# Performance work log

Measured on AMD Instinct MI355X. Metric: run time of the kernel, lower is better.

Reference implementation:

```python
import jax, jax.numpy as jnp
import numpy as np
from jax import lax

L, H, C, V, BLK = 6, 12, 768, 50257, 1024
B, T = 4, 1024
HD = C // H
EPS = 1e-5


def _norm(key, shape, scale=0.02):
    return jax.random.normal(key, shape, dtype=jnp.float32) * scale


def setup_inputs() -> dict:
    key = jax.random.key(0)
    ks = jax.random.split(key, 16)
    idx = jax.random.randint(ks[0], (B, T), 0, V)
    inp = {
        "idx": idx,
        "wte": _norm(ks[1], (V, C)),
        "wpe": _norm(ks[2], (BLK, C)),
        "ln1_s": jnp.ones((L, C)),
        "ln1_b": jnp.zeros((L, C)),
        "qkv_w": _norm(ks[3], (L, C, 3 * C)),
        "qkv_b": jnp.zeros((L, 3 * C)),
        "proj_w": _norm(ks[4], (L, C, C)),
        "proj_b": jnp.zeros((L, C)),
        "ln2_s": jnp.ones((L, C)),
        "ln2_b": jnp.zeros((L, C)),
        "fc_w": _norm(ks[5], (L, C, 4 * C)),
        "fc_b": jnp.zeros((L, 4 * C)),
        "fcp_w": _norm(ks[6], (L, 4 * C, C)),
        "fcp_b": jnp.zeros((L, C)),
        "lnf_s": jnp.ones((C,)),
        "lnf_b": jnp.zeros((C,)),
    }
    return inp


def layer_norm(x, s, b):
    mu = jnp.mean(x, axis=-1, keepdims=True)
    var = jnp.mean(jnp.square(x - mu), axis=-1, keepdims=True)
    return (x - mu) * lax.rsqrt(var + EPS) * s + b


def block(x, p):
    ln1_s, ln1_b, qkv_w, qkv_b, proj_w, proj_b, ln2_s, ln2_b, fc_w, fc_b, fcp_w, fcp_b = p
    Bx, Tx, Cx = x.shape
    h = layer_norm(x, ln1_s, ln1_b)
    qkv = h @ qkv_w + qkv_b  # [B,T,3C]
    q, k, v = jnp.split(qkv, 3, axis=-1)
    q = q.reshape(Bx, Tx, H, HD).swapaxes(1, 2)  # [B,H,T,hd]
    k = k.reshape(Bx, Tx, H, HD).swapaxes(1, 2)
    v = v.reshape(Bx, Tx, H, HD).swapaxes(1, 2)
    attn = jnp.einsum("bhqd,bhkd->bhqk", q, k) / jnp.sqrt(jnp.float32(HD))
    mask = jnp.tril(jnp.ones((Tx, Tx), dtype=bool))
    attn = jnp.where(mask, attn, -jnp.inf)
    attn = jax.nn.softmax(attn, axis=-1)
    y = jnp.einsum("bhqk,bhkd->bhqd", attn, v)
    y = y.swapaxes(1, 2).reshape(Bx, Tx, Cx)
    x = x + (y @ proj_w + proj_b)
    h = layer_norm(x, ln2_s, ln2_b)
    h = jax.nn.gelu(h @ fc_w + fc_b, approximate=True)
    x = x + (h @ fcp_w + fcp_b)
    return x


def reference(idx, wte, wpe, ln1_s, ln1_b, qkv_w, qkv_b, proj_w, proj_b,
              ln2_s, ln2_b, fc_w, fc_b, fcp_w, fcp_b, lnf_s, lnf_b):
    Tx = idx.shape[1]
    x = wte[idx] + wpe[:Tx][None]  # [B,T,C]
    params = (ln1_s, ln1_b, qkv_w, qkv_b, proj_w, proj_b,
              ln2_s, ln2_b, fc_w, fc_b, fcp_w, fcp_b)
    def step(carry, p):
        return block(carry, p), None
    x, _ = lax.scan(step, x, params)
    x = layer_norm(x, lnf_s, lnf_b)
    logits = x @ wte.T  # tied embedding attend
    return logits
```

## Files before the change

### kernel.cpp

```cpp
#include <hip/hip_runtime.h>
#include <math.h>

#define LNUM 6
#define HNUM 12
#define CDIM 768
#define VDIM 50257
#define BDIM 4
#define TDIM 1024
#define NTOK 4096

typedef __bf16 bf16;
typedef __bf16 bf16x8 __attribute__((ext_vector_type(8)));
typedef float  floatx4 __attribute__((ext_vector_type(4)));
typedef unsigned int u32;

__device__ inline void gload16(const bf16* gsrc, bf16* lds) {
  __builtin_amdgcn_global_load_lds(
      (const __attribute__((address_space(1))) u32*)gsrc,
      (__attribute__((address_space(3))) u32*)lds, 16, 0, 0);
}

__global__ void k_cvt_bf16(const float* __restrict__ in, bf16* __restrict__ out, long n) {
  long i = ((long)blockIdx.x * blockDim.x + threadIdx.x) * 4;
  long stride = (long)gridDim.x * blockDim.x * 4;
  for (; i < n; i += stride) {
    float4 v = *reinterpret_cast<const float4*>(in + i);
    bf16 b0 = (bf16)v.x, b1 = (bf16)v.y, b2 = (bf16)v.z, b3 = (bf16)v.w;
    ushort4 pk;
    pk.x = __builtin_bit_cast(unsigned short, b0);
    pk.y = __builtin_bit_cast(unsigned short, b1);
    pk.z = __builtin_bit_cast(unsigned short, b2);
    pk.w = __builtin_bit_cast(unsigned short, b3);
    *reinterpret_cast<ushort4*>(out + i) = pk;
  }
}

#define TILES_QKV  1728
#define TILES_PROJ 576
#define TILES_FC   2304
#define TILES_FCP  2304
#define TILES_LAYER (TILES_QKV + TILES_PROJ + TILES_FC + TILES_FCP)

__global__ __launch_bounds__(256) void k_trans_all(
    const float* __restrict__ qkv_w, const float* __restrict__ proj_w,
    const float* __restrict__ fc_w, const float* __restrict__ fcp_w,
    bf16* __restrict__ wq, bf16* __restrict__ wp,
    bf16* __restrict__ wf, bf16* __restrict__ wfp) {
  __shared__ float tile[32][33];
  int bid = blockIdx.x;
  int layer = bid / TILES_LAYER, r = bid % TILES_LAYER;
  const float* src; bf16* dst; int K, N, tx, ty;
  if (r < TILES_QKV) {
    src = qkv_w + (size_t)layer * CDIM * 3 * CDIM; dst = wq + (size_t)layer * CDIM * 3 * CDIM;
    K = CDIM; N = 3 * CDIM; tx = r % 72; ty = r / 72;
  } else if (r < TILES_QKV + TILES_PROJ) {
    r -= TILES_QKV;
    src = proj_w + (size_t)layer * CDIM * CDIM; dst = wp + (size_t)layer * CDIM * CDIM;
    K = CDIM; N = CDIM; tx = r % 24; ty = r / 24;
  } else if (r < TILES_QKV + TILES_PROJ + TILES_FC) {
    r -= TILES_QKV + TILES_PROJ;
    src = fc_w + (size_t)layer * CDIM * 4 * CDIM; dst = wf + (size_t)layer * CDIM * 4 * CDIM;
    K = CDIM; N = 4 * CDIM; tx = r % 96; ty = r / 96;
  } else {
    r -= TILES_QKV + TILES_PROJ + TILES_FC;
    src = fcp_w + (size_t)layer * 4 * CDIM * CDIM; dst = wfp + (size_t)layer * 4 * CDIM * CDIM;
    K = 4 * CDIM; N = CDIM; tx = r % 24; ty = r / 24;
  }
  int n0 = tx * 32, k0 = ty * 32;
  int nx = threadIdx.x & 31, tyy = threadIdx.x >> 5;
  #pragma unroll
  for (int p = 0; p < 4; ++p) {
    int k = tyy + p * 8;
    tile[k][nx] = src[(size_t)(k0 + k) * N + n0 + nx];
  }
  __syncthreads();
  #pragma unroll
  for (int p = 0; p < 4; ++p) {
    int n = tyy + p * 8;
    dst[(size_t)(n0 + n) * K + k0 + nx] = (bf16)tile[nx][n];
  }
}

__global__ void k_embed(const int* __restrict__ idx, const float* __restrict__ wte,
                        const float* __restrict__ wpe, float* __restrict__ x) {
  int tok = blockIdx.x;
  int t = tok & (TDIM - 1);
  int id = idx[tok];
  const float* a = wte + (size_t)id * CDIM;
  const float* p = wpe + (size_t)t * CDIM;
  float* o = x + (size_t)tok * CDIM;
  for (int c = threadIdx.x; c < CDIM; c += 256) o[c] = a[c] + p[c];
}

__global__ __launch_bounds__(256) void k_layernorm(const float* __restrict__ x,
    const float* __restrict__ sc, const float* __restrict__ bi, bf16* __restrict__ out) {
  __shared__ float red[8];
  int row = blockIdx.x;
  const float* xr = x + (size_t)row * CDIM;
  int t = threadIdx.x;
  float v0 = xr[t], v1 = xr[t + 256], v2 = xr[t + 512];
  float s = v0 + v1 + v2;
  #pragma unroll
  for (int o = 32; o > 0; o >>= 1) s += __shfl_down(s, o);
  if ((t & 63) == 0) red[t >> 6] = s;
  __syncthreads();
  float mean = (red[0] + red[1] + red[2] + red[3]) * (1.0f / CDIM);
  float d0 = v0 - mean, d1 = v1 - mean, d2 = v2 - mean;
  float q = d0 * d0 + d1 * d1 + d2 * d2;
  #pragma unroll
  for (int o = 32; o > 0; o >>= 1) q += __shfl_down(q, o);
  if ((t & 63) == 0) red[4 + (t >> 6)] = q;
  __syncthreads();
  float var = (red[4] + red[5] + red[6] + red[7]) * (1.0f / CDIM);
  float rs = rsqrtf(var + 1e-5f);
  bf16* orow = out + (size_t)row * CDIM;
  orow[t]       = (bf16)(d0 * rs * sc[t]       + bi[t]);
  orow[t + 256] = (bf16)(d1 * rs * sc[t + 256] + bi[t + 256]);
  orow[t + 512] = (bf16)(d2 * rs * sc[t + 512] + bi[t + 512]);
}

__device__ inline float gelu_f(float x) {
  float x3 = x * x * x;
  return 0.5f * x * (1.0f + tanhf(0.7978845608028654f * (x + 0.044715f * x3)));
}

template<int TBM, int EPI>
__global__ __launch_bounds__(512, 1) void k_gemm8(
    const bf16* __restrict__ A, const bf16* __restrict__ Bt,
    const float* __restrict__ bias,
    float* __restrict__ Cf, bf16* __restrict__ Cb,
    int N, int K) {
  constexpr int MI = TBM / 32;
  constexpr int MH = MI / 2;
  constexpr int MTILES = 4096 / TBM;
  __shared__ __align__(16) bf16 smem[2 * 8192 + 2 * TBM * 32];
  bf16* Bs = smem;
  bf16* As = smem + 2 * 8192;
  const int nwg = gridDim.x;
  const int id = blockIdx.x;
  const int swz = (id & 7) * (nwg >> 3) + (id >> 3);
  const int m0 = (swz % MTILES) * TBM;
  const int n0 = (swz / MTILES) * 256;
  const int tid = threadIdx.x, lane = tid & 63, wave = tid >> 6;
  const int wr = wave >> 2, wc = wave & 3;
  const int g = lane >> 4, r16 = lane & 15;
  const int numK = K >> 5;
  const int wsl = wave * 512;

  const int srow = wave * 16 + (lane >> 2);
  const int scol = ((lane & 3) ^ ((lane >> 3) & 3)) * 8;
  const bf16* at  = A  + (size_t)(m0 + srow) * K + scol;
  const bf16* at1 = A  + (size_t)(m0 + srow + 128) * K + scol;
  const bf16* bt  = Bt + (size_t)(n0 + srow) * K + scol;
  const bf16* bt1 = Bt + (size_t)(n0 + srow + 128) * K + scol;
  const int sw = (g ^ ((r16 >> 1) & 3)) * 8;
  const int a_off = (wr * (TBM / 2) + r16) * 32 + sw;
  const int b_off = (wc * 64 + r16) * 32 + sw;

  floatx4 acc[MI][4] = {};

#define STB(s0, s1, pb) do { gload16((s0), Bs + (pb) * 8192 + wsl); \
                             gload16((s1), Bs + (pb) * 8192 + wsl + 4096); } while (0)
#define STA(s0, s1, pb) do { gload16((s0), As + (pb) * TBM * 32 + wsl); \
                             if constexpr (TBM == 256) gload16((s1), As + (pb) * TBM * 32 + wsl + 4096); } while (0)

  STB(bt, bt1, 0);
  STA(at, at1, 0);
  STB(bt + 32, bt1 + 32, 1);
  asm volatile("s_waitcnt vmcnt(2)" ::: "memory");
  __builtin_amdgcn_s_barrier();

  for (int t = 0; t < numK; ++t) {
    const int p = t & 1, pn = p ^ 1;
    bf16x8 af[MH], bfr[4];

    #pragma unroll
    for (int j = 0; j < 4; ++j) bfr[j] = *(const bf16x8*)&Bs[p * 8192 + b_off + j * 512];
    #pragma unroll
    for (int i = 0; i < MH; ++i) af[i] = *(const bf16x8*)&As[p * TBM * 32 + a_off + i * 512];
    if (t + 1 < numK) STA(at + 32, at1 + 32, pn);
    __builtin_amdgcn_s_barrier();
    asm volatile("s_waitcnt lgkmcnt(0)" ::: "memory");
    __builtin_amdgcn_s_setprio(1);
    #pragma unroll
    for (int i = 0; i < MH; ++i)
      #pragma unroll
      for (int j = 0; j < 4; ++j)
        acc[i][j] = __builtin_amdgcn_mfma_f32_16x16x32_bf16(af[i], bfr[j], acc[i][j], 0, 0, 0);
    __builtin_amdgcn_s_setprio(0);
    __builtin_amdgcn_s_barrier();

    #pragma unroll
    for (int i = 0; i < MH; ++i) af[i] = *(const bf16x8*)&As[p * TBM * 32 + a_off + (i + MH) * 512];
    if (t + 2 < numK) STB(bt + 64, bt1 + 64, p);
    __builtin_amdgcn_s_barrier();
    asm volatile("s_waitcnt lgkmcnt(0)" ::: "memory");
    __builtin_amdgcn_s_setprio(1);
    #pragma unroll
    for (int i = 0; i < MH; ++i)
      #pragma unroll
      for (int j = 0; j < 4; ++j)
        acc[i + MH][j] = __builtin_amdgcn_mfma_f32_16x16x32_bf16(af[i], bfr[j], acc[i + MH][j], 0, 0, 0);
    __builtin_amdgcn_s_setprio(0);
    if (t + 2 < numK) { asm volatile("s_waitcnt vmcnt(2)" ::: "memory"); }
    else              { asm volatile("s_waitcnt vmcnt(0)" ::: "memory"); }
    __builtin_amdgcn_s_barrier();

    at += 32; at1 += 32; bt += 32; bt1 += 32;
  }
#undef STB
#undef STA

  if (EPI == 0) {
    float* sb = reinterpret_cast<float*>(smem) + wave * 1088;
    const int seg = lane & 15, rq = lane >> 4;
    const int mrow_base = m0 + wr * (TBM / 2);
    const int ncol_base = n0 + wc * 64;
    #pragma unroll
    for (int mf = 0; mf < MI; ++mf) {
      #pragma unroll
      for (int nf = 0; nf < 4; ++nf) {
        #pragma unroll
        for (int q = 0; q < 4; ++q)
          sb[(g * 4 + q) * 68 + nf * 16 + r16] = acc[mf][nf][q];
      }
      #pragma unroll
      for (int pz = 0; pz < 4; ++pz) {
        int row = rq + pz * 4;
        floatx4 v = *reinterpret_cast<const floatx4*>(&sb[row * 68 + seg * 4]);
        int m = mrow_base + mf * 16 + row;
        int n = ncol_base + seg * 4;
        if (n + 4 <= N) {
          __builtin_memcpy(&Cf[(size_t)m * N + n], &v, 16);
        } else {
          #pragma unroll
          for (int e = 0; e < 4; ++e)
            if (n + e < N) Cf[(size_t)m * N + n + e] = v[e];
        }
      }
    }
  } else {
    bf16* sb = smem + wave * 1152;
    const int rr_rd = lane & 15, seg = lane >> 4;
    const int nb = n0 + wc * 64 + r16;
    float bv[4];
    #pragma unroll
    for (int j = 0; j < 4; ++j) bv[j] = bias[nb + j * 16];
    #pragma unroll
    for (int mf = 0; mf < MI; ++mf) {
      #pragma unroll
      for (int j = 0; j < 4; ++j) {
        #pragma unroll
        for (int q = 0; q < 4; ++q) {
          float v = acc[mf][j][q] + bv[j];
          if (EPI == 3) v = gelu_f(v);
          sb[(g * 4 + q) * 72 + j * 16 + r16] = (bf16)v;
        }
      }
      bf16x8 o0 = *(const bf16x8*)&sb[rr_rd * 72 + seg * 16];
      bf16x8 o1 = *(const bf16x8*)&sb[rr_rd * 72 + seg * 16 + 8];
      size_t orow = (size_t)(m0 + wr * (TBM / 2) + mf * 16 + rr_rd) * N + (n0 + wc * 64 + seg * 16);
      *(bf16x8*)&Cb[orow] = o0;
      *(bf16x8*)&Cb[orow + 8] = o1;
    }
  }
}

template<int TBM, int MI, int NI, int EPI>
__global__ __launch_bounds__(256) void k_gemm(
    const bf16* __restrict__ A, const bf16* __restrict__ Bt,
    const float* __restrict__ bias, const float* __restrict__ resid,
    float* __restrict__ Cf, bf16* __restrict__ Cb,
    int M, int N, int K) {
  constexpr int BN = 128;
  constexpr int WGN = BN / (NI * 16);
  constexpr int AI = TBM / 32;
  constexpr int BI = BN / 32;
  __shared__ __align__(16) bf16 As[TBM * 64];
  __shared__ __align__(16) bf16 Bs[BN * 64];
  const int m0 = blockIdx.x * TBM, n0 = blockIdx.y * BN;
  const int tid = threadIdx.x;
  const int lane = tid & 63, wave = tid >> 6;
  const int wr = wave / WGN, wc = wave % WGN;
  const int l8 = lane >> 3, s8 = lane & 7;
  const int g = lane >> 4, r16 = lane & 15;

  floatx4 acc[MI][NI] = {};

  const bf16* a_src = A + (size_t)(m0 + l8) * K + s8 * 8;
  const bf16* b_src = Bt + (size_t)(n0 + l8) * K + s8 * 8;

  for (int k0 = 0; k0 < K; k0 += 64) {
    #pragma unroll
    for (int t = 0; t < AI; ++t) {
      int row0 = wave * (TBM / 4) + t * 8;
      gload16(a_src + (size_t)row0 * K + k0, &As[row0 * 64]);
    }
    #pragma unroll
    for (int t = 0; t < BI; ++t) {
      int row0 = wave * 32 + t * 8;
      gload16(b_src + (size_t)row0 * K + k0, &Bs[row0 * 64]);
    }
    __syncthreads();
    #pragma unroll
    for (int kk = 0; kk < 2; ++kk) {
      bf16x8 af[MI], bfr[NI];
      #pragma unroll
      for (int i = 0; i < MI; ++i)
        af[i] = *reinterpret_cast<const bf16x8*>(&As[(wr * MI * 16 + i * 16 + r16) * 64 + g * 8 + kk * 32]);
      #pragma unroll
      for (int j = 0; j < NI; ++j)
        bfr[j] = *reinterpret_cast<const bf16x8*>(&Bs[(wc * NI * 16 + j * 16 + r16) * 64 + g * 8 + kk * 32]);
      #pragma unroll
      for (int i = 0; i < MI; ++i) {
        #pragma unroll
        for (int j = 0; j < NI; ++j)
          acc[i][j] = __builtin_amdgcn_mfma_f32_16x16x32_bf16(af[i], bfr[j], acc[i][j], 0, 0, 0);
      }
    }
    __syncthreads();
  }

  int mb = m0 + wr * MI * 16 + g * 4;
  int nb = n0 + wc * NI * 16 + r16;
  #pragma unroll
  for (int j = 0; j < NI; ++j) {
    int n = nb + j * 16;
    if (n >= N) continue;
    float bv = (EPI >= 2) ? bias[n] : 0.0f;
    #pragma unroll
    for (int i = 0; i < MI; ++i) {
      #pragma unroll
      for (int q = 0; q < 4; ++q) {
        int m = mb + i * 16 + q;
        float v = acc[i][j][q] + bv;
        size_t o = (size_t)m * N + n;
        if (EPI == 2)      Cf[o] = v + resid[o];
        else if (EPI == 3) Cb[o] = (bf16)gelu_f(v);
        else if (EPI == 4) Cb[o] = (bf16)v;
        else               Cf[o] = v;
      }
    }
  }
}

__global__ __launch_bounds__(256) void k_vtrans(const bf16* __restrict__ qkv, bf16* __restrict__ vt) {
  __shared__ bf16 tile[64][72];
  int bh = blockIdx.x, t0 = blockIdx.y * 64;
  int b = bh / HNUM, h = bh % HNUM;
  int tid = threadIdx.x;
  int r8 = tid >> 3, s8 = tid & 7;
  #pragma unroll
  for (int p = 0; p < 2; ++p) {
    int row = p * 32 + r8;
    uint4 v = *reinterpret_cast<const uint4*>(
        qkv + (size_t)(b * TDIM + t0 + row) * (3 * CDIM) + 2 * CDIM + h * 64 + s8 * 8);
    *reinterpret_cast<uint4*>(&tile[row][s8 * 8]) = v;
  }
  __syncthreads();
  int d = tid >> 2, q4 = tid & 3;
  #pragma unroll
  for (int half = 0; half < 2; ++half) {
    int t = q4 * 16 + half * 8;
    bf16x8 o;
    #pragma unroll
    for (int u = 0; u < 8; ++u) o[u] = tile[t + u][d];
    *reinterpret_cast<bf16x8*>(vt + (size_t)bh * (64 * TDIM) + (size_t)d * TDIM + t0 + t) = o;
  }
}

__global__ __launch_bounds__(256) void k_attn(const bf16* __restrict__ qkv,
                                              const bf16* __restrict__ vt,
                                              bf16* __restrict__ y) {
  __shared__ __align__(16) bf16 Ks[64 * 64];
  __shared__ __align__(16) bf16 Vs[64 * 64];
  __shared__ __align__(16) bf16 Ps[64 * 64];
  const int bh = blockIdx.x, qt = blockIdx.y;
  const int b = bh / HNUM, h = bh % HNUM;
  const int tid = threadIdx.x, lane = tid & 63, wave = tid >> 6;
  const int g = lane >> 4, r16 = lane & 15;
  const int w16 = wave * 16;
  const int r8 = tid >> 3, s8 = tid & 7;

  bf16x8 qf[2];
  {
    const bf16* qsrc = qkv + (size_t)(b * TDIM + qt * 64 + w16 + r16) * (3 * CDIM) + h * 64 + g * 8;
    qf[0] = *reinterpret_cast<const bf16x8*>(qsrc);
    qf[1] = *reinterpret_cast<const bf16x8*>(qsrc + 32);
  }

  float m_r[4], l_r[4];
  floatx4 yacc[4] = {};
  #pragma unroll
  for (int q = 0; q < 4; ++q) { m_r[q] = -1e30f; l_r[q] = 0.f; }

  for (int kt = 0; kt <= qt; ++kt) {
    __syncthreads();
    #pragma unroll
    for (int p = 0; p < 2; ++p) {
      int row = p * 32 + r8;
      uint4 kv = *reinterpret_cast<const uint4*>(
          qkv + (size_t)(b * TDIM + kt * 64 + row) * (3 * CDIM) + CDIM + h * 64 + s8 * 8);
      *reinterpret_cast<uint4*>(&Ks[row * 64 + ((s8 ^ (row & 7)) * 8)]) = kv;
      uint4 vv = *reinterpret_cast<const uint4*>(
          vt + (size_t)bh * (64 * TDIM) + (size_t)row * TDIM + kt * 64 + s8 * 8);
      *reinterpret_cast<uint4*>(&Vs[row * 64 + ((s8 ^ (row & 7)) * 8)]) = vv;
    }
    __syncthreads();

    floatx4 sa[4] = {};
    #pragma unroll
    for (int c = 0; c < 2; ++c) {
      bf16x8 kf[4];
      #pragma unroll
      for (int j = 0; j < 4; ++j) {
        int krow = j * 16 + r16;
        kf[j] = *reinterpret_cast<const bf16x8*>(&Ks[krow * 64 + (((g + 4 * c) ^ (krow & 7)) * 8)]);
      }
      #pragma unroll
      for (int j = 0; j < 4; ++j)
        sa[j] = __builtin_amdgcn_mfma_f32_16x16x32_bf16(qf[c], kf[j], sa[j], 0, 0, 0);
    }

    const bool diag = (kt == qt);
    float p_v[4][4];
    #pragma unroll
    for (int q = 0; q < 4; ++q) {
      int qrow = w16 + g * 4 + q;
      float mx = -1e30f;
      #pragma unroll
      for (int j = 0; j < 4; ++j) {
        float s = sa[j][q] * 0.125f;
        if (diag && (r16 + j * 16) > qrow) s = -1e30f;
        p_v[j][q] = s;
        mx = fmaxf(mx, s);
      }
      #pragma unroll
      for (int o = 1; o < 16; o <<= 1) mx = fmaxf(mx, __shfl_xor(mx, o));
      float mnew = fmaxf(m_r[q], mx);
      float ps = 0.f;
      #pragma unroll
      for (int j = 0; j < 4; ++j) {
        float p = __expf(p_v[j][q] - mnew);
        p_v[j][q] = p;
        ps += p;
      }
      #pragma unroll
      for (int o = 1; o < 16; o <<= 1) ps += __shfl_xor(ps, o);
      float alpha = __expf(m_r[q] - mnew);
      m_r[q] = mnew;
      l_r[q] = l_r[q] * alpha + ps;
      #pragma unroll
      for (int j = 0; j < 4; ++j) yacc[j][q] *= alpha;
      #pragma unroll
      for (int j = 0; j < 4; ++j) {
        int col = r16 + j * 16;
        Ps[qrow * 64 + (col ^ ((qrow & 7) << 3))] = (bf16)p_v[j][q];
      }
    }

    #pragma unroll
    for (int ks = 0; ks < 2; ++ks) {
      int prow = w16 + r16;
      bf16x8 pa = *reinterpret_cast<const bf16x8*>(&Ps[prow * 64 + (((g + 4 * ks) ^ (prow & 7)) * 8)]);
      #pragma unroll
      for (int j = 0; j < 4; ++j) {
        int vrow = j * 16 + r16;
        bf16x8 vb = *reinterpret_cast<const bf16x8*>(&Vs[vrow * 64 + (((g + 4 * ks) ^ (vrow & 7)) * 8)]);
        yacc[j] = __builtin_amdgcn_mfma_f32_16x16x32_bf16(pa, vb, yacc[j], 0, 0, 0);
      }
    }
  }

  #pragma unroll
  for (int q = 0; q < 4; ++q) {
    float inv = 1.0f / l_r[q];
    int tok = b * TDIM + qt * 64 + w16 + g * 4 + q;
    #pragma unroll
    for (int j = 0; j < 4; ++j)
      y[(size_t)tok * CDIM + h * 64 + r16 + j * 16] = (bf16)(yacc[j][q] * inv);
  }
}

extern "C" void kernel_launch(void* const* d_in, const int* in_sizes, int n_in,
                              void* d_out, int out_size, void* d_ws, size_t ws_size,
                              hipStream_t stream) {
  (void)in_sizes; (void)n_in; (void)out_size;
  const int*   idx    = (const int*)  d_in[0];
  const float* wte    = (const float*)d_in[1];
  const float* wpe    = (const float*)d_in[2];
  const float* ln1_s  = (const float*)d_in[3];
  const float* ln1_b  = (const float*)d_in[4];
  const float* qkv_w  = (const float*)d_in[5];
  const float* qkv_b  = (const float*)d_in[6];
  const float* proj_w = (const float*)d_in[7];
  const float* proj_b = (const float*)d_in[8];
  const float* ln2_s  = (const float*)d_in[9];
  const float* ln2_b  = (const float*)d_in[10];
  const float* fc_w   = (const float*)d_in[11];
  const float* fc_b   = (const float*)d_in[12];
  const float* fcp_w  = (const float*)d_in[13];
  const float* fcp_b  = (const float*)d_in[14];
  const float* lnf_s  = (const float*)d_in[15];
  const float* lnf_b  = (const float*)d_in[16];
  float* logits = (float*)d_out;

  char* base = (char*)d_ws;
  size_t off = 0;
  auto alloc = [&](size_t bytes) -> void* {
    void* p = base + off;
    off += (bytes + 255) & ~(size_t)255;
    return p;
  };
  bf16*  wte_bf  = (bf16*) alloc((size_t)VDIM * CDIM * 2);
  bf16*  wq_all  = (bf16*) alloc((size_t)LNUM * 3 * CDIM * CDIM * 2);
  bf16*  wp_all  = (bf16*) alloc((size_t)LNUM * CDIM * CDIM * 2);
  bf16*  wf_all  = (bf16*) alloc((size_t)LNUM * 4 * CDIM * CDIM * 2);
  bf16*  wfp_all = (bf16*) alloc((size_t)LNUM * 4 * CDIM * CDIM * 2);
  float* x       = (float*)alloc((size_t)NTOK * CDIM * 4);
  bf16*  hb      = (bf16*) alloc((size_t)NTOK * CDIM * 2);
  bf16*  qkv_bf  = (bf16*) alloc((size_t)NTOK * 3 * CDIM * 2);
  bf16*  vt      = (bf16*) alloc((size_t)BDIM * HNUM * 64 * TDIM * 2);
  bf16*  yb      = (bf16*) alloc((size_t)NTOK * CDIM * 2);
  bf16*  gb      = (bf16*) alloc((size_t)NTOK * 4 * CDIM * 2);
  if (off > ws_size) return;

  k_cvt_bf16<<<4096, 256, 0, stream>>>(wte, wte_bf, (long)VDIM * CDIM);
  k_trans_all<<<LNUM * TILES_LAYER, 256, 0, stream>>>(qkv_w, proj_w, fc_w, fcp_w,
                                                      wq_all, wp_all, wf_all, wfp_all);
  k_embed<<<NTOK, 256, 0, stream>>>(idx, wte, wpe, x);

  for (int l = 0; l < LNUM; ++l) {
    const bf16* wq  = wq_all  + (size_t)l * 3 * CDIM * CDIM;
    const bf16* wp  = wp_all  + (size_t)l * CDIM * CDIM;
    const bf16* wf  = wf_all  + (size_t)l * 4 * CDIM * CDIM;
    const bf16* wfp = wfp_all + (size_t)l * 4 * CDIM * CDIM;

    k_layernorm<<<NTOK, 256, 0, stream>>>(x, ln1_s + l*CDIM, ln1_b + l*CDIM, hb);
    k_gemm8<128,4><<<32 * 9, 512, 0, stream>>>(hb, wq, qkv_b + (size_t)l*3*CDIM, nullptr, qkv_bf, 3*CDIM, CDIM);
    k_vtrans<<<dim3(BDIM*HNUM, TDIM/64), 256, 0, stream>>>(qkv_bf, vt);
    k_attn<<<dim3(BDIM*HNUM, TDIM/64), 256, 0, stream>>>(qkv_bf, vt, yb);
    k_gemm<64,4,2,2><<<dim3(NTOK/64, 6), 256, 0, stream>>>(yb, wp, proj_b + (size_t)l*CDIM, x, x, nullptr, NTOK, CDIM, CDIM);
    k_layernorm<<<NTOK, 256, 0, stream>>>(x, ln2_s + l*CDIM, ln2_b + l*CDIM, hb);
    k_gemm8<128,3><<<32 * 12, 512, 0, stream>>>(hb, wf, fc_b + (size_t)l*4*CDIM, nullptr, gb, 4*CDIM, CDIM);
    k_gemm<64,4,2,2><<<dim3(NTOK/64, 6), 256, 0, stream>>>(gb, wfp, fcp_b + (size_t)l*CDIM, x, x, nullptr, NTOK, CDIM, 4*CDIM);
  }

  k_layernorm<<<NTOK, 256, 0, stream>>>(x, lnf_s, lnf_b, hb);
  int ntile = (VDIM + 255) / 256;
  k_gemm8<256,0><<<16 * ntile, 512, 0, stream>>>(hb, wte_bf, nullptr, logits, nullptr, VDIM, CDIM);
}
```

Measured before the change: 1.779 ms.

## Add dedicated logits GEMM with deeper multi-stage LDS pipeline and nontemporal stores

Adds a specialized kernel for the vocab-projection GEMM. It uses a 4-deep ring for B tiles and a 3-deep ring for A tiles in LDS, with loads issued further ahead, and writes the fp32 logits with nontemporal stores to avoid polluting cache. The EPI==0 path is removed from the generic gemm8 template. The aim is to hide global-load latency on the largest GEMM and to reduce cache pressure from the large logits output, at the cost of more LDS (112KB) and more complex waitcnt bookkeeping.

```diff
diff --git a/kernel.cpp b/kernel.cpp
--- a/kernel.cpp
+++ b/kernel.cpp
@@ -124,6 +124,119 @@
   return 0.5f * x * (1.0f + tanhf(0.7978845608028654f * (x + 0.044715f * x3)));
 }
 
+__global__ __launch_bounds__(512, 1) void k_gemm_logits(
+    const bf16* __restrict__ A, const bf16* __restrict__ Bt,
+    float* __restrict__ Cf, int N, int K) {
+  __shared__ __align__(16) bf16 smem[7 * 8192];
+  bf16* Bs = smem;
+  bf16* As = smem + 4 * 8192;
+  const int nwg = gridDim.x;
+  const int id = blockIdx.x;
+  const int swz = (id & 7) * (nwg >> 3) + (id >> 3);
+  const int m0 = (swz & 15) * 256;
+  const int n0 = (swz >> 4) * 256;
+  const int tid = threadIdx.x, lane = tid & 63, wave = tid >> 6;
+  const int wr = wave >> 2, wc = wave & 3;
+  const int g = lane >> 4, r16 = lane & 15;
+  const int numK = K >> 5;
+  const int wsl = wave * 512;
+
+  const int srow = wave * 16 + (lane >> 2);
+  const int scol = ((lane & 3) ^ ((lane >> 3) & 3)) * 8;
+  const bf16* at  = A  + (size_t)(m0 + srow) * K + scol;
+  const bf16* at1 = A  + (size_t)(m0 + srow + 128) * K + scol;
+  const bf16* bt  = Bt + (size_t)(n0 + srow) * K + scol;
+  const bf16* bt1 = Bt + (size_t)(n0 + srow + 128) * K + scol;
+  const int sw = (g ^ ((r16 >> 1) & 3)) * 8;
+  const int a_off = (wr * 128 + r16) * 32 + sw;
+  const int b_off = (wc * 64 + r16) * 32 + sw;
+
+  floatx4 acc[8][4] = {};
+
+#define STBd(s0, s1, pb) do { gload16((s0), Bs + (pb) * 8192 + wsl); \
+                              gload16((s1), Bs + (pb) * 8192 + wsl + 4096); } while (0)
+#define STAd(s0, s1, pb) do { gload16((s0), As + (pb) * 8192 + wsl); \
+                              gload16((s1), As + (pb) * 8192 + wsl + 4096); } while (0)
+
+  STBd(bt,      bt1,      0);
+  STAd(at,      at1,      0);
+  STBd(bt + 32, bt1 + 32, 1);
+  STAd(at + 32, at1 + 32, 1);
+  STBd(bt + 64, bt1 + 64, 2);
+  asm volatile("s_waitcnt vmcnt(6)" ::: "memory");
+  __builtin_amdgcn_s_barrier();
+
+  for (int t = 0; t < numK; ++t) {
+    const int ab = t % 3, bb = t & 3;
+    bf16x8 af[4], bfr[4];
+
+    #pragma unroll
+    for (int j = 0; j < 4; ++j) bfr[j] = *(const bf16x8*)&Bs[bb * 8192 + b_off + j * 512];
+    #pragma unroll
+    for (int i = 0; i < 4; ++i) af[i] = *(const bf16x8*)&As[ab * 8192 + a_off + i * 512];
+    if (t + 2 < numK) STAd(at + 64, at1 + 64, (t + 2) % 3);
+    __builtin_amdgcn_s_barrier();
+    asm volatile("s_waitcnt lgkmcnt(0)" ::: "memory");
+    __builtin_amdgcn_s_setprio(1);
+    #pragma unroll
+    for (int i = 0; i < 4; ++i)
+      #pragma unroll
+      for (int j = 0; j < 4; ++j)
+        acc[i][j] = __builtin_amdgcn_mfma_f32_16x16x32_bf16(af[i], bfr[j], acc[i][j], 0, 0, 0);
+    __builtin_amdgcn_s_setprio(0);
+    __builtin_amdgcn_s_barrier();
+
+    #pragma unroll
+    for (int i = 0; i < 4; ++i) af[i] = *(const bf16x8*)&As[ab * 8192 + a_off + (i + 4) * 512];
+    if (t + 3 < numK) STBd(bt + 96, bt1 + 96, (t + 3) & 3);
+    __builtin_amdgcn_s_barrier();
+    asm volatile("s_waitcnt lgkmcnt(0)" ::: "memory");
+    __builtin_amdgcn_s_setprio(1);
+    #pragma unroll
+    for (int i = 0; i < 4; ++i)
+      #pragma unroll
+      for (int j = 0; j < 4; ++j)
+        acc[i + 4][j] = __builtin_amdgcn_mfma_f32_16x16x32_bf16(af[i], bfr[j], acc[i + 4][j], 0, 0, 0);
+    __builtin_amdgcn_s_setprio(0);
+    if (t + 3 < numK)      { asm volatile("s_waitcnt vmcnt(6)" ::: "memory"); }
+    else if (t + 2 < numK) { asm volatile("s_waitcnt vmcnt(4)" ::: "memory"); }
+    else                   { asm volatile("s_waitcnt vmcnt(0)" ::: "memory"); }
+    __builtin_amdgcn_s_barrier();
+
+    at += 32; at1 += 32; bt += 32; bt1 += 32;
+  }
+#undef STBd
+#undef STAd
+
+  float* sb = reinterpret_cast<float*>(smem) + wave * 1088;
+  const int seg = lane & 15, rq = lane >> 4;
+  const int mrow_base = m0 + wr * 128;
+  const int ncol_base = n0 + wc * 64;
+  #pragma unroll
+  for (int mf = 0; mf < 8; ++mf) {
+    #pragma unroll
+    for (int nf = 0; nf < 4; ++nf) {
+      #pragma unroll
+      for (int q = 0; q < 4; ++q)
+        sb[(g * 4 + q) * 68 + nf * 16 + r16] = acc[mf][nf][q];
+    }
+    #pragma unroll
+    for (int pz = 0; pz < 4; ++pz) {
+      int row = rq + pz * 4;
+      floatx4 v = *reinterpret_cast<const floatx4*>(&sb[row * 68 + seg * 4]);
+      int m = mrow_base + mf * 16 + row;
+      int n = ncol_base + seg * 4;
+      if (n + 4 <= N) {
+        __builtin_nontemporal_store(v, reinterpret_cast<floatx4*>(&Cf[(size_t)m * N + n]));
+      } else {
+        #pragma unroll
+        for (int e = 0; e < 4; ++e)
+          if (n + e < N) Cf[(size_t)m * N + n + e] = v[e];
+      }
+    }
+  }
+}
+
 template<int TBM, int EPI>
 __global__ __launch_bounds__(512, 1) void k_gemm8(
     const bf16* __restrict__ A, const bf16* __restrict__ Bt,
@@ -211,58 +324,28 @@
 #undef STB
 #undef STA
 
-  if (EPI == 0) {
-    float* sb = reinterpret_cast<float*>(smem) + wave * 1088;
-    const int seg = lane & 15, rq = lane >> 4;
-    const int mrow_base = m0 + wr * (TBM / 2);
-    const int ncol_base = n0 + wc * 64;
-    #pragma unroll
-    for (int mf = 0; mf < MI; ++mf) {
-      #pragma unroll
-      for (int nf = 0; nf < 4; ++nf) {
-        #pragma unroll
-        for (int q = 0; q < 4; ++q)
-          sb[(g * 4 + q) * 68 + nf * 16 + r16] = acc[mf][nf][q];
-      }
-      #pragma unroll
-      for (int pz = 0; pz < 4; ++pz) {
-        int row = rq + pz * 4;
-        floatx4 v = *reinterpret_cast<const floatx4*>(&sb[row * 68 + seg * 4]);
-        int m = mrow_base + mf * 16 + row;
-        int n = ncol_base + seg * 4;
-        if (n + 4 <= N) {
-          __builtin_memcpy(&Cf[(size_t)m * N + n], &v, 16);
-        } else {
-          #pragma unroll
-          for (int e = 0; e < 4; ++e)
-            if (n + e < N) Cf[(size_t)m * N + n + e] = v[e];
-        }
-      }
-    }
-  } else {
-    bf16* sb = smem + wave * 1152;
-    const int rr_rd = lane & 15, seg = lane >> 4;
-    const int nb = n0 + wc * 64 + r16;
-    float bv[4];
-    #pragma unroll
-    for (int j = 0; j < 4; ++j) bv[j] = bias[nb + j * 16];
-    #pragma unroll
-    for (int mf = 0; mf < MI; ++mf) {
-      #pragma unroll
-      for (int j = 0; j < 4; ++j) {
-        #pragma unroll
-        for (int q = 0; q < 4; ++q) {
-          float v = acc[mf][j][q] + bv[j];
-          if (EPI == 3) v = gelu_f(v);
-          sb[(g * 4 + q) * 72 + j * 16 + r16] = (bf16)v;
-        }
-      }
-      bf16x8 o0 = *(const bf16x8*)&sb[rr_rd * 72 + seg * 16];
-      bf16x8 o1 = *(const bf16x8*)&sb[rr_rd * 72 + seg * 16 + 8];
-      size_t orow = (size_t)(m0 + wr * (TBM / 2) + mf * 16 + rr_rd) * N + (n0 + wc * 64 + seg * 16);
-      *(bf16x8*)&Cb[orow] = o0;
-      *(bf16x8*)&Cb[orow + 8] = o1;
-    }
+  bf16* sb = smem + wave * 1152;
+  const int rr_rd = lane & 15, seg = lane >> 4;
+  const int nb = n0 + wc * 64 + r16;
+  float bv[4];
+  #pragma unroll
+  for (int j = 0; j < 4; ++j) bv[j] = bias[nb + j * 16];
+  #pragma unroll
+  for (int mf = 0; mf < MI; ++mf) {
+    #pragma unroll
+    for (int j = 0; j < 4; ++j) {
+      #pragma unroll
+      for (int q = 0; q < 4; ++q) {
+        float v = acc[mf][j][q] + bv[j];
+        if (EPI == 3) v = gelu_f(v);
+        sb[(g * 4 + q) * 72 + j * 16 + r16] = (bf16)v;
+      }
+    }
+    bf16x8 o0 = *(const bf16x8*)&sb[rr_rd * 72 + seg * 16];
+    bf16x8 o1 = *(const bf16x8*)&sb[rr_rd * 72 + seg * 16 + 8];
+    size_t orow = (size_t)(m0 + wr * (TBM / 2) + mf * 16 + rr_rd) * N + (n0 + wc * 64 + seg * 16);
+    *(bf16x8*)&Cb[orow] = o0;
+    *(bf16x8*)&Cb[orow + 8] = o1;
   }
 }
 
@@ -548,5 +631,5 @@
 
   k_layernorm<<<NTOK, 256, 0, stream>>>(x, lnf_s, lnf_b, hb);
   int ntile = (VDIM + 255) / 256;
-  k_gemm8<256,0><<<16 * ntile, 512, 0, stream>>>(hb, wte_bf, nullptr, logits, nullptr, VDIM, CDIM);
-}
+  k_gemm_logits<<<16 * ntile, 512, 0, stream>>>(hb, wte_bf, logits, VDIM, CDIM);
+}
```

Result: slower. 1.827 ms (+2.7%).
